# Performance work log

Measured on AMD Instinct MI355X. Metric: run time of the kernel, lower is better.

Reference implementation:

```python
import jax, jax.numpy as jnp
import numpy as np

DEPTH = 10
LEAF = 2 ** DEPTH          # 1024 leaves
NODE_NUM = 2 * LEAF - 1    # 2047
N = NODE_NUM + 1           # 2048 nodes incl. global node 0
ATTN = 4
D = 128
B = 8
L = 2


def _trace_children(ni):
    terms = []
    s, e = ni << 1, (ni << 1) | 1
    while s <= NODE_NUM and e <= NODE_NUM:
        terms.extend(range(s, e + 1))
        s <<= 1
        e = (e << 1) | 1
    return terms


def _trace_left(si):
    ni, cd, terms, stop = si + LEAF, DEPTH, [], False
    while not stop:
        cs = ni - ATTN + 1 - ((ni - ATTN + 1) & 1)
        stop = cs < 2 ** cd
        cs = max(2 ** cd, cs)
        terms.extend(range(cs, ni + 1))
        ni = (cs - 1) >> 1
        cd -= 1
    return terms


def _trace_right(ei):
    ni, cd, terms, stop = ei + LEAF, DEPTH, [], False
    while not stop:
        ce = ni + ATTN - 1 + ((ni - ATTN) & 1)
        stop = ce >= 2 ** (cd + 1)
        ce = min(2 ** (cd + 1) - 1, ce)
        terms.extend(range(ni, ce + 1))
        ni = (ce + 1) >> 1
        cd -= 1
    return terms


def _build_edges():
    src, dst = [], []
    for ni in range(1, NODE_NUM + 1):
        if ni < LEAF:
            t = _trace_children(ni)
        else:
            t = _trace_left(ni - LEAF) + _trace_right(ni - LEAF)
        src.extend(t)
        dst.extend([ni] * len(t))
    e = np.stack([np.asarray(src, np.int64), np.asarray(dst, np.int64)])  # [2, E]
    off = np.arange(B, dtype=np.int64) * N
    eb = (e[:, None, :] + off[None, :, None]).reshape(2, -1)  # batch-offset like _fetch_edge_data
    return eb.astype(np.int32)


def setup_inputs() -> dict:
    key = jax.random.key(0)
    k0, k1, k2 = jax.random.split(key, 3)
    s = 1.0 / np.sqrt(D)
    return {
        "elements": jax.random.normal(k0, (B, LEAF, D), jnp.float32),
        "ln_gamma": jnp.ones((L, D), jnp.float32),
        "ln_beta": jnp.zeros((L, D), jnp.float32),
        "w_nei": (jax.random.normal(k1, (L, D, D), jnp.float32) * s),
        "b_nei": jnp.zeros((L, D), jnp.float32),
        "w_root": (jax.random.normal(k2, (L, D, D), jnp.float32) * s),
        "edge_index": jnp.asarray(_build_edges()),
    }


def _sinusoid(pos, d):
    # ArbitraryPositionEncoder: sinusoidal encoding over (possibly negative) positions
    half = d // 2
    inv = jnp.exp(-jnp.arange(half, dtype=jnp.float32) * (np.log(10000.0) / half))
    ang = pos[:, None] * inv[None, :]  # [n, half]
    return jnp.stack([jnp.sin(ang), jnp.cos(ang)], -1).reshape(pos.shape[0], d)


def reference(elements, ln_gamma, ln_beta, w_nei, b_nei, w_root, edge_index):
    Bx, leaf, d = elements.shape
    depth = int(np.log2(leaf))
    # bottom-up tree compression (mean of two children)
    cur = elements
    levels = [cur]
    for _ in range(depth):
        cur = 0.5 * (cur[:, 0::2] + cur[:, 1::2])
        levels.append(cur)
    # node ordering: [global node 0 (=-1), root (level 0), ..., leaves (level depth)]
    node_feat = jnp.concatenate(
        [jnp.full((Bx, 1, d), -1.0, elements.dtype)] + levels[::-1], axis=1)  # [B, N, D]
    n = node_feat.shape[1]
    # positional encoding: vertical = floor(log2(idx)), horizontal = idx - 2^vertical
    idx = jnp.arange(n, dtype=jnp.float32)
    vpos = jnp.floor(jnp.log2(jnp.where(idx == 0, 0.5, idx)))
    hpos = idx - jnp.exp2(vpos)
    enc = jnp.concatenate([_sinusoid(hpos, d // 2), _sinusoid(vpos, d // 2)], -1)  # [N, D]
    x = (node_feat + enc[None]).reshape(Bx * n, d)
    src, dst = edge_index[0], edge_index[1]
    nseg = Bx * n
    deg = jnp.maximum(
        jax.ops.segment_sum(jnp.ones(src.shape, jnp.float32), dst, num_segments=nseg), 1.0)
    # DeepGCNLayer res+ blocks with SAGEConv (mean aggr)
    for l in range(ln_gamma.shape[0]):
        mu = jnp.mean(x, -1, keepdims=True)
        var = jnp.mean((x - mu) ** 2, -1, keepdims=True)
        h = (x - mu) * jax.lax.rsqrt(var + 1e-5) * ln_gamma[l] + ln_beta[l]
        h = jax.nn.gelu(h, approximate=False)
        agg = jax.ops.segment_sum(h[src], dst, num_segments=nseg) / deg[:, None]
        h = agg @ w_nei[l] + b_nei[l] + h @ w_root[l]
        x = x + h
    return x.reshape(Bx, n, d)
```

## Files before the change

### kernel.cpp

```cpp
#include <hip/hip_runtime.h>
#include <hip/hip_bf16.h>

#define LEAFN 1024
#define NN    2048
#define BATCH 8
#define DD    128
#define ROWS  (BATCH*NN)
#define AHS   384
#define NB    256
#define NT    1024

#define LOG1E4_OVER_32 0.28782313662425575f

#define SLACK 9
#define CSTRIDE 136
#define AGGL_OFF 54672
#define RED_OFF  63376
#define RED2_OFF 64400

typedef __bf16 bf16x8 __attribute__((ext_vector_type(8)));
typedef float  floatx4 __attribute__((ext_vector_type(4)));
typedef float  floatx2 __attribute__((ext_vector_type(2)));

__device__ __forceinline__ float bf2f(unsigned short u) {
  return __uint_as_float(((unsigned)u) << 16);
}
__device__ __forceinline__ unsigned short f2bf(float f) {
  unsigned u = __float_as_uint(f);
  u += 0x7FFFu + ((u >> 16) & 1u);
  return (unsigned short)(u >> 16);
}
__device__ __forceinline__ float gelu(float v) {
  return 0.5f * v * (1.0f + erff(v * 0.70710678118f));
}
__device__ __forceinline__ floatx2 bfpair(unsigned u) {
  floatx2 r;
  r[0] = __uint_as_float(u << 16);
  r[1] = __uint_as_float(u & 0xffff0000u);
  return r;
}

__device__ __forceinline__ float enc_val(int node, int d) {
  float hp, vp;
  if (node == 0) { hp = -0.5f; vp = -1.0f; }
  else {
    int v = 31 - __clz(node);
    hp = (float)(node - (1 << v));
    vp = (float)v;
  }
  float pos = (d < 64) ? hp : vp;
  int i = ((d < 64) ? d : (d - 64)) >> 1;
  float inv = __expf(-(float)i * LOG1E4_OVER_32);
  float ang = pos * inv;
  return (d & 1) ? __cosf(ang) : __sinf(ang);
}

__device__ __forceinline__ void win_cd(int jb, int cd, int& lo_, int& wd_) {
  int g0 = 1024 + jb * 32, g1 = g0 + 31;
  int a0 = g0 >> (10 - cd), a1 = g1 >> (10 - cd);
  int l = a0 - SLACK, h = a1 + SLACK;
  int lvlo = 1 << cd, lvhi = (2 << cd) - 1;
  lo_ = l < lvlo ? lvlo : l;
  int hh = h > lvhi ? lvhi : h;
  int w = hh - lo_ + 1;
  wd_ = w < 0 ? 0 : w;
}

__device__ __forceinline__ void gbarN(int* bar, int slot) {
  __syncthreads();
  if (threadIdx.x == 0) {
    int g = blockIdx.x & 7;
    int* base = bar + (slot * 8 + g) * 64;
    __threadfence();
    if (__hip_atomic_fetch_add(base, 1, __ATOMIC_RELAXED,
                               __HIP_MEMORY_SCOPE_AGENT) == 31)
      __hip_atomic_store(base + 32, 1, __ATOMIC_RELAXED,
                         __HIP_MEMORY_SCOPE_AGENT);
    while (!__hip_atomic_load(base + 32, __ATOMIC_RELAXED,
                              __HIP_MEMORY_SCOPE_AGENT))
      __builtin_amdgcn_s_sleep(1);
    __threadfence();
  }
  __syncthreads();
}

__device__ __forceinline__ void ph_tree(char* smemc, int b, int s,
                                        const float* __restrict__ elements,
                                        float* __restrict__ x,
                                        float* __restrict__ lvl4,
                                        unsigned short* __restrict__ ah,
                                        const float* __restrict__ gamma,
                                        const float* __restrict__ beta,
                                        float* __restrict__ sroot,
                                        float* xci, int* bar) {
  float* sm = (float*)smemc;
  floatx4* smv = (floatx4*)smemc;
  int tid = threadIdx.x;
  const float4* src = (const float4*)(elements + (size_t)(b * LEAFN + s * 64) * DD);
  for (int i = tid; i < 2048; i += NT) {
    int f = i * 4;
    int j = f >> 7, d = f & 127;
    *(float4*)&sm[(63 + j) * DD + d] = src[i];
  }
  __syncthreads();
  for (int lv = 5; lv >= 0; --lv) {
    int nodes = 1 << lv;
    for (int idx = tid; idx < nodes * 32; idx += NT) {
      int k = nodes + (idx >> 5);
      int j = idx & 31;
      smv[(k - 1) * 32 + j] = 0.5f * (smv[(2 * k - 1) * 32 + j] + smv[(2 * k) * 32 + j]);
    }
    __syncthreads();
  }
  if (tid < 32) ((floatx4*)&lvl4[(size_t)(b * 16 + s) * DD])[tid] = smv[tid];
  __syncthreads();
  if (tid == 0) {
    __threadfence();
    __hip_atomic_store(bar + 1536 + b * 64 + s * 4, 1, __ATOMIC_RELAXED,
                       __HIP_MEMORY_SCOPE_AGENT);
  }
  {
    int d2 = tid & 63;
    int i = d2 & 31;
    float inv = __expf(-(float)i * LOG1E4_OVER_32);
    bool lowhalf = d2 < 32;
    for (int idx2 = tid; idx2 < 127 * 64; idx2 += NT) {
      int row = idx2 >> 6;
      int k = row + 1;
      int lv = 31 - __clz(k);
      int g = ((16 + s) << lv) | (k - (1 << lv));
      float vp = (float)(lv + 4);
      float hp = (float)(g - (16 << lv));
      float pos = lowhalf ? hp : vp;
      float sv, cv;
      __sincosf(pos * inv, &sv, &cv);
      int base = row * DD + 2 * d2;
      float xv0 = sm[base] + sv;
      float xv1 = sm[base + 1] + cv;
      sm[base] = xv0; sm[base + 1] = xv1;
      if (k >= 64 || k <= 32) {
        float2 o = make_float2(xv0, xv1);
        *(float2*)&x[((size_t)(b * NN + g)) * DD + 2 * d2] = o;
      }
    }
  }
  __syncthreads();
  {
    int wave = tid >> 6, lane = tid & 63;
    if (wave >= 8) {
      int wl = wave & 7;
      int mt = wl >> 2, nq = wl & 3;
      int m = lane & 15, q = lane >> 4;
#pragma unroll
      for (int ci = 0; ci < 2; ++ci)
#pragma unroll
        for (int r = 0; r < 4; ++r) {
          int t = 32 + mt * 16 + q * 4 + r;
          int k = (t == 63) ? 1 : t + 1;
          int d = (nq * 2 + ci) * 16 + m;
          xci[ci * 4 + r] = sm[(k - 1) * DD + d];
        }
    }
  }
  __syncthreads();
  {
    int sub = tid & 7, dp = sub * 16;
    for (int rr = tid >> 3; rr < 127; rr += NT / 8) {
      float* rowp = &sm[rr * DD + dp];
      float4 q0 = *(float4*)rowp;
      float4 q1 = *(float4*)(rowp + 4);
      float4 q2 = *(float4*)(rowp + 8);
      float4 q3 = *(float4*)(rowp + 12);
      float v[16] = {q0.x, q0.y, q0.z, q0.w, q1.x, q1.y, q1.z, q1.w,
                     q2.x, q2.y, q2.z, q2.w, q3.x, q3.y, q3.z, q3.w};
      float s1 = 0.f, s2 = 0.f;
#pragma unroll
      for (int j = 0; j < 16; ++j) { s1 += v[j]; s2 += v[j] * v[j]; }
      s1 += __shfl_xor(s1, 1); s2 += __shfl_xor(s2, 1);
      s1 += __shfl_xor(s1, 2); s2 += __shfl_xor(s2, 2);
      s1 += __shfl_xor(s1, 4); s2 += __shfl_xor(s2, 4);
      float mu = s1 * (1.0f / 128.0f);
      float var = s2 * (1.0f / 128.0f) - mu * mu;
      float rinv = rsqrtf(var + 1e-5f);
      int k = rr + 1, lv = 31 - __clz(k);
      int g = ((16 + s) << lv) | (k - (1 << lv));
      __attribute__((aligned(16))) unsigned short o[16];
      float hv[16];
#pragma unroll
      for (int j = 0; j < 16; ++j) {
        hv[j] = gelu((v[j] - mu) * rinv * gamma[dp + j] + beta[dp + j]);
        o[j] = f2bf(hv[j]);
      }
      *(float4*)rowp        = make_float4(hv[0], hv[1], hv[2], hv[3]);
      *(float4*)(rowp + 4)  = make_float4(hv[4], hv[5], hv[6], hv[7]);
      *(float4*)(rowp + 8)  = make_float4(hv[8], hv[9], hv[10], hv[11]);
      *(float4*)(rowp + 12) = make_float4(hv[12], hv[13], hv[14], hv[15]);
      unsigned short* dst = &ah[(size_t)(b * NN + g) * AHS + 128 + dp];
      *(uint4*)&dst[0] = *(uint4*)&o[0];
      *(uint4*)&dst[8] = *(uint4*)&o[8];
    }
  }
  __syncthreads();
  for (int lv = 5; lv >= 0; --lv) {
    int nk = 1 << lv;
    float inv = 1.0f / (float)((1 << (7 - lv)) - 2);
    for (int idx = tid; idx < nk * 32; idx += NT) {
      int k = nk + (idx >> 5);
      int j = idx & 31;
      floatx4 S = smv[(2 * k - 1) * 32 + j] + smv[(2 * k) * 32 + j];
      if (lv < 5) S = S + smv[(4 * k - 1) * 32 + j] + smv[(4 * k + 1) * 32 + j];
      smv[(2 * k - 1) * 32 + j] = S;
      int g = ((16 + s) << lv) | (k - nk);
      ushort4 o;
      o.x = f2bf(S[0] * inv); o.y = f2bf(S[1] * inv);
      o.z = f2bf(S[2] * inv); o.w = f2bf(S[3] * inv);
      *(ushort4*)&ah[(size_t)(b * NN + g) * AHS + j * 4] = o;
    }
    __syncthreads();
  }
  if (tid < 32)
    ((floatx4*)&sroot[(size_t)(b * 16 + s) * DD])[tid] = smv[32 + tid];
}

__device__ __forceinline__ void ph_top(char* smemc, int b,
                                       const float* __restrict__ lvl4,
                                       unsigned short* __restrict__ ah,
                                       const float* __restrict__ gamma,
                                       const float* __restrict__ beta) {
  float (*xs)[DD] = (float(*)[DD])smemc;
  int tid = threadIdx.x;
  if (tid < 128) {
    int d = tid;
    float v[16];
    for (int j = 0; j < 16; ++j) v[j] = lvl4[(b * 16 + j) * DD + d];
    for (int j = 0; j < 8; ++j) v[j] = 0.5f * (v[2 * j] + v[2 * j + 1]);
    for (int j = 0; j < 8; ++j) xs[8 + j][d] = v[j] + enc_val(8 + j, d);
    for (int j = 0; j < 4; ++j) v[j] = 0.5f * (v[2 * j] + v[2 * j + 1]);
    for (int j = 0; j < 4; ++j) xs[4 + j][d] = v[j] + enc_val(4 + j, d);
    for (int j = 0; j < 2; ++j) v[j] = 0.5f * (v[2 * j] + v[2 * j + 1]);
    for (int j = 0; j < 2; ++j) xs[2 + j][d] = v[j] + enc_val(2 + j, d);
    v[0] = 0.5f * (v[0] + v[1]);
    xs[1][d] = v[0] + enc_val(1, d);
    xs[0][d] = -1.0f + enc_val(0, d);
  }
  __syncthreads();
  if (tid < 128) {
    int rr = tid >> 3, sub = tid & 7, dp = sub * 16;
    float w[16], s1 = 0.f, s2 = 0.f;
#pragma unroll
    for (int j = 0; j < 16; ++j) { w[j] = xs[rr][dp + j]; s1 += w[j]; s2 += w[j] * w[j]; }
    s1 += __shfl_xor(s1, 1); s2 += __shfl_xor(s2, 1);
    s1 += __shfl_xor(s1, 2); s2 += __shfl_xor(s2, 2);
    s1 += __shfl_xor(s1, 4); s2 += __shfl_xor(s2, 4);
    float mu = s1 * (1.0f / 128.0f);
    float var = s2 * (1.0f / 128.0f) - mu * mu;
    float rinv = rsqrtf(var + 1e-5f);
    __attribute__((aligned(16))) unsigned short o[16];
#pragma unroll
    for (int j = 0; j < 16; ++j)
      o[j] = f2bf(gelu((w[j] - mu) * rinv * gamma[dp + j] + beta[dp + j]));
    unsigned short* dst = &ah[(size_t)(b * NN + rr) * AHS + 128 + dp];
    *(uint4*)&dst[0] = *(uint4*)&o[0];
    *(uint4*)&dst[8] = *(uint4*)&o[8];
  }
  __syncthreads();
}

__device__ __forceinline__ void ph_aggsub(char* smemc, int b, int s,
                                          unsigned short* ah,
                                          float* __restrict__ sroot) {
  floatx4 (*S)[32] = (floatx4(*)[32])smemc;
  int tid = threadIdx.x;
  for (int idx = tid; idx < 32 * 32; idx += NT) {
    int k = 32 + (idx >> 5), q = idx & 31;
    int c = (16 + s) * 64 + (2 * k - 64);
    size_t a0 = (size_t)(b * NN + c) * AHS + 256 + q * 4;
    ushort4 u0 = *(const ushort4*)&ah[a0];
    ushort4 u1 = *(const ushort4*)&ah[a0 + AHS];
    floatx4 v;
    v[0] = bf2f(u0.x) + bf2f(u1.x);
    v[1] = bf2f(u0.y) + bf2f(u1.y);
    v[2] = bf2f(u0.z) + bf2f(u1.z);
    v[3] = bf2f(u0.w) + bf2f(u1.w);
    S[k][q] = v;
    int g = (16 + s) * 32 + (k - 32);
    int r = b * NN + g;
    ushort4 o;
    o.x = f2bf(v[0] * 0.5f); o.y = f2bf(v[1] * 0.5f);
    o.z = f2bf(v[2] * 0.5f); o.w = f2bf(v[3] * 0.5f);
    *(ushort4*)&ah[(size_t)r * AHS + q * 4] = o;
  }
  __syncthreads();
  for (int lv = 4; lv >= 0; --lv) {
    int nk = 1 << lv;
    float inv = 1.0f / (float)((1 << (7 - lv)) - 2);
    for (int idx = tid; idx < nk * 32; idx += NT) {
      int k = nk + (idx >> 5), q = idx & 31;
      int c = ((16 + s) << (lv + 1)) | (2 * k - 2 * nk);
      size_t a0 = (size_t)(b * NN + c) * AHS + 256 + q * 4;
      ushort4 u0 = *(const ushort4*)&ah[a0];
      ushort4 u1 = *(const ushort4*)&ah[a0 + AHS];
      floatx4 sc0 = S[2 * k][q], sc1 = S[2 * k + 1][q];
      floatx4 v;
      v[0] = bf2f(u0.x) + bf2f(u1.x) + sc0[0] + sc1[0];
      v[1] = bf2f(u0.y) + bf2f(u1.y) + sc0[1] + sc1[1];
      v[2] = bf2f(u0.z) + bf2f(u1.z) + sc0[2] + sc1[2];
      v[3] = bf2f(u0.w) + bf2f(u1.w) + sc0[3] + sc1[3];
      S[k][q] = v;
      int g = ((16 + s) << lv) | (k - nk);
      int r = b * NN + g;
      ushort4 o;
      o.x = f2bf(v[0] * inv); o.y = f2bf(v[1] * inv);
      o.z = f2bf(v[2] * inv); o.w = f2bf(v[3] * inv);
      *(ushort4*)&ah[(size_t)r * AHS + q * 4] = o;
    }
    __syncthreads();
  }
  for (int q = tid; q < 32; q += NT)
    ((floatx4*)sroot)[(size_t)(b * 16 + s) * 32 + q] = S[1][q];
}

__device__ __forceinline__ void ph_leafagg(char* smemc, int b, int jb,
                                           const int* __restrict__ srcv,
                                           const int* __restrict__ s0a,
                                           const int* __restrict__ s1a,
                                           const unsigned short* __restrict__ eoff,
                                           unsigned short* ah, int hoff) {
  unsigned short* cache = (unsigned short*)smemc;
  int tid = threadIdx.x;
  int lo[11], wd[11], off[11];
  int acc_off = 0;
#pragma unroll
  for (int cd = 10; cd >= 1; --cd) {
    win_cd(jb, cd, lo[cd], wd[cd]);
    off[cd] = acc_off;
    acc_off += wd[cd];
  }
#pragma unroll
  for (int cd = 10; cd >= 1; --cd) {
    int w = wd[cd];
    for (int t = tid; t < w * 16; t += NT) {
      int row = t >> 4, seg = t & 15;
      *(uint4*)&cache[(off[cd] + row) * CSTRIDE + seg * 8] =
          *(const uint4*)&ah[(size_t)(b * NN + lo[cd] + row) * AHS + hoff + seg * 8];
    }
  }
  __syncthreads();

  int leaf = tid >> 5, half = (tid >> 4) & 1, c = tid & 15;
  int r = b * NN + 1024 + jb * 32 + leaf;
  int e0 = s0a[r], e1 = s1a[r];
  int n = e1 - e0;
  int mid = e0 + (n >> 1);
  int ebeg = half ? mid : e0;
  int eend = half ? e1 : mid;
  int cb = c * 16;
  floatx2 a0 = {0.f, 0.f}, a1 = {0.f, 0.f}, a2 = {0.f, 0.f}, a3 = {0.f, 0.f};
  auto one = [&](int ei) {
    unsigned o = eoff[ei];
    uint4 u;
    if (o != 0xFFFFu)
      u = *(const uint4*)(smemc + o + cb);
    else {
      int g = srcv[ei] - b * NN;
      u = *(const uint4*)&ah[(size_t)(b * NN + g) * AHS + hoff + c * 8];
    }
    a0 += bfpair(u.x); a1 += bfpair(u.y); a2 += bfpair(u.z); a3 += bfpair(u.w);
  };
  int e = ebeg;
  for (; e + 4 <= eend; e += 4) {
    unsigned o0 = eoff[e], o1 = eoff[e + 1], o2 = eoff[e + 2], o3 = eoff[e + 3];
    if (!((((o0 + 1) | (o1 + 1) | (o2 + 1) | (o3 + 1)) >> 16))) {
      uint4 u0 = *(const uint4*)(smemc + o0 + cb);
      uint4 u1 = *(const uint4*)(smemc + o1 + cb);
      uint4 u2 = *(const uint4*)(smemc + o2 + cb);
      uint4 u3 = *(const uint4*)(smemc + o3 + cb);
      a0 += bfpair(u0.x); a1 += bfpair(u0.y); a2 += bfpair(u0.z); a3 += bfpair(u0.w);
      a0 += bfpair(u1.x); a1 += bfpair(u1.y); a2 += bfpair(u1.z); a3 += bfpair(u1.w);
      a0 += bfpair(u2.x); a1 += bfpair(u2.y); a2 += bfpair(u2.z); a3 += bfpair(u2.w);
      a0 += bfpair(u3.x); a1 += bfpair(u3.y); a2 += bfpair(u3.z); a3 += bfpair(u3.w);
    } else {
      one(e); one(e + 1); one(e + 2); one(e + 3);
    }
  }
  for (; e < eend; ++e) one(e);
  a0[0] += __shfl_xor(a0[0], 16); a0[1] += __shfl_xor(a0[1], 16);
  a1[0] += __shfl_xor(a1[0], 16); a1[1] += __shfl_xor(a1[1], 16);
  a2[0] += __shfl_xor(a2[0], 16); a2[1] += __shfl_xor(a2[1], 16);
  a3[0] += __shfl_xor(a3[0], 16); a3[1] += __shfl_xor(a3[1], 16);
  if (!half) {
    float inv = 1.0f / (float)max(n, 1);
    unsigned short* aggl = (unsigned short*)(smemc + AGGL_OFF);
    __attribute__((aligned(16))) unsigned short o[8];
    o[0] = f2bf(a0[0] * inv); o[1] = f2bf(a0[1] * inv);
    o[2] = f2bf(a1[0] * inv); o[3] = f2bf(a1[1] * inv);
    o[4] = f2bf(a2[0] * inv); o[5] = f2bf(a2[1] * inv);
    o[6] = f2bf(a3[0] * inv); o[7] = f2bf(a3[1] * inv);
    *(uint4*)&aggl[leaf * CSTRIDE + c * 8] = *(uint4*)&o[0];
  }
}

__device__ __forceinline__ void ph_topfin(int b,
                                          const float* __restrict__ sroot,
                                          unsigned short* ah, int hoff) {
  int d = threadIdx.x;
  float S16[16], h16[16], Sv[16];
#pragma unroll
  for (int j = 0; j < 16; ++j) S16[j] = sroot[(size_t)(b * 16 + j) * DD + d];
#pragma unroll
  for (int j = 0; j < 16; ++j)
    h16[j] = bf2f(ah[(size_t)(b * NN + 16 + j) * AHS + hoff + d]);
#pragma unroll
  for (int k = 8; k < 16; ++k)
    Sv[k] = h16[2 * k - 16] + h16[2 * k - 15] + S16[2 * k - 16] + S16[2 * k - 15];
#pragma unroll
  for (int k = 7; k >= 1; --k)
    Sv[k] = bf2f(ah[(size_t)(b * NN + 2 * k) * AHS + hoff + d]) +
            bf2f(ah[(size_t)(b * NN + 2 * k + 1) * AHS + hoff + d]) +
            Sv[2 * k] + Sv[2 * k + 1];
#pragma unroll
  for (int k = 1; k < 16; ++k) {
    int dv = 31 - __clz(k);
    float inv = 1.0f / (float)((1 << (11 - dv)) - 2);
    ah[(size_t)(b * NN + k) * AHS + d] = f2bf(Sv[k] * inv);
  }
  ah[(size_t)(b * NN) * AHS + d] = f2bf(0.0f);
}

__device__ __forceinline__ void ph_gemm32(char* redc, const unsigned short* aggl,
                                          int rowbase, unsigned short* ah,
                                          const unsigned short* __restrict__ wfl,
                                          const float* __restrict__ bn,
                                          float* __restrict__ x, int hoff_in,
                                          const float* __restrict__ gamma,
                                          const float* __restrict__ beta,
                                          float* xc, int first_layer) {
  int wave = threadIdx.x >> 6, lane = threadIdx.x & 63;
  bool act = wave < 8;
  int wl = wave & 7;
  int mt = wl >> 2, nq = wl & 3;
  int r0 = rowbase + mt * 16;
  int m = lane & 15, q = lane >> 4;
  floatx4 acc[2];
  acc[0] = (floatx4){0.f, 0.f, 0.f, 0.f};
  acc[1] = (floatx4){0.f, 0.f, 0.f, 0.f};
  if (act) {
    const unsigned short* arow = ah + (size_t)(r0 + m) * AHS + q * 8;
    const bf16x8* B = (const bf16x8*)wfl + lane;
#pragma unroll
    for (int kc = 0; kc < 8; ++kc) {
      bf16x8 a0;
      if (kc < 4)
        a0 = *(const bf16x8*)&aggl[(mt * 16 + m) * CSTRIDE + kc * 32 + q * 8];
      else
        a0 = *(const bf16x8*)(arow + hoff_in + (kc - 4) * 32);
#pragma unroll
      for (int ci = 0; ci < 2; ++ci) {
        bf16x8 bb = B[(kc * 8 + nq * 2 + ci) * 64];
        acc[ci] = __builtin_amdgcn_mfma_f32_16x16x32_bf16(a0, bb, acc[ci], 0, 0, 0);
      }
    }
  }
  if (first_layer) {
    float s1[4] = {0.f, 0.f, 0.f, 0.f}, s2[4] = {0.f, 0.f, 0.f, 0.f};
    if (act) {
#pragma unroll
      for (int ci = 0; ci < 2; ++ci) {
        int col = (nq * 2 + ci) * 16 + m;
        float bias = bn[col];
#pragma unroll
        for (int r = 0; r < 4; ++r) {
          int row = r0 + q * 4 + r;
          float v = x[(size_t)row * DD + col] + acc[ci][r] + bias;
          xc[ci * 4 + r] = v;
          s1[r] += v; s2[r] += v * v;
        }
      }
#pragma unroll
      for (int r = 0; r < 4; ++r) {
        s1[r] += __shfl_xor(s1[r], 1); s2[r] += __shfl_xor(s2[r], 1);
        s1[r] += __shfl_xor(s1[r], 2); s2[r] += __shfl_xor(s2[r], 2);
        s1[r] += __shfl_xor(s1[r], 4); s2[r] += __shfl_xor(s2[r], 4);
        s1[r] += __shfl_xor(s1[r], 8); s2[r] += __shfl_xor(s2[r], 8);
      }
    }
    float* red = (float*)redc;
    int rl = mt * 16 + q * 4;
    __syncthreads();
    if (act && m == 0) {
#pragma unroll
      for (int r = 0; r < 4; ++r) {
        red[(rl + r) * 4 + nq] = s1[r];
        red[128 + (rl + r) * 4 + nq] = s2[r];
      }
    }
    __syncthreads();
    if (act) {
      float mu[4], rv[4];
#pragma unroll
      for (int r = 0; r < 4; ++r) {
        float t1 = red[(rl + r) * 4] + red[(rl + r) * 4 + 1] +
                   red[(rl + r) * 4 + 2] + red[(rl + r) * 4 + 3];
        float t2 = red[128 + (rl + r) * 4] + red[128 + (rl + r) * 4 + 1] +
                   red[128 + (rl + r) * 4 + 2] + red[128 + (rl + r) * 4 + 3];
        mu[r] = t1 * (1.0f / 128.0f);
        float var = t2 * (1.0f / 128.0f) - mu[r] * mu[r];
        rv[r] = rsqrtf(var + 1e-5f);
      }
#pragma unroll
      for (int ci = 0; ci < 2; ++ci) {
        int col = (nq * 2 + ci) * 16 + m;
        float gm = gamma[col], bt = beta[col];
#pragma unroll
        for (int r = 0; r < 4; ++r) {
          int row = r0 + q * 4 + r;
          float hh = gelu((xc[ci * 4 + r] - mu[r]) * rv[r] * gm + bt);
          ah[(size_t)row * AHS + 256 + col] = f2bf(hh);
        }
      }
    }
  } else {
    if (act) {
#pragma unroll
      for (int ci = 0; ci < 2; ++ci) {
        int col = (nq * 2 + ci) * 16 + m;
        float bias = bn[col];
#pragma unroll
        for (int r = 0; r < 4; ++r) {
          int row = r0 + q * 4 + r;
          x[(size_t)row * DD + col] = xc[ci * 4 + r] + acc[ci][r] + bias;
        }
      }
    }
  }
}

__device__ __forceinline__ void ph_gemm32s(char* redc, int b, int sb, int tbase,
                                           unsigned short* ah,
                                           const unsigned short* __restrict__ wfl,
                                           const float* __restrict__ bn,
                                           float* __restrict__ x, int hoff_in,
                                           const float* __restrict__ gamma,
                                           const float* __restrict__ beta,
                                           float* xc, int first_layer,
                                           const float* __restrict__ gx) {
  int wave = threadIdx.x >> 6, lane = threadIdx.x & 63;
  bool act = wave >= 8;
  int wl = wave & 7;
  int mt = wl >> 2, nq = wl & 3;
  int m = lane & 15, q = lane >> 4;
  int tA = tbase + mt * 16 + m;
  int kA = (tA == 63) ? 1 : tA + 1;
  int lvA = 31 - __clz(kA);
  int rowA = b * NN + (((16 + sb) << lvA) | (kA - (1 << lvA)));
  int rowO[4];
#pragma unroll
  for (int r = 0; r < 4; ++r) {
    int t = tbase + mt * 16 + q * 4 + r;
    int k = (t == 63) ? 1 : t + 1;
    int lv = 31 - __clz(k);
    rowO[r] = b * NN + (((16 + sb) << lv) | (k - (1 << lv)));
  }
  floatx4 acc[2];
  acc[0] = (floatx4){0.f, 0.f, 0.f, 0.f};
  acc[1] = (floatx4){0.f, 0.f, 0.f, 0.f};
  if (act) {
    const unsigned short* arow = ah + (size_t)rowA * AHS + q * 8;
    const bf16x8* B = (const bf16x8*)wfl + lane;
#pragma unroll
    for (int kc = 0; kc < 8; ++kc) {
      int koff = (kc < 4) ? kc * 32 : hoff_in + (kc - 4) * 32;
      bf16x8 a0 = *(const bf16x8*)(arow + koff);
#pragma unroll
      for (int ci = 0; ci < 2; ++ci) {
        bf16x8 bb = B[(kc * 8 + nq * 2 + ci) * 64];
        acc[ci] = __builtin_amdgcn_mfma_f32_16x16x32_bf16(a0, bb, acc[ci], 0, 0, 0);
      }
    }
  }
  if (first_layer) {
    float s1[4] = {0.f, 0.f, 0.f, 0.f}, s2[4] = {0.f, 0.f, 0.f, 0.f};
    if (act) {
#pragma unroll
      for (int ci = 0; ci < 2; ++ci) {
        int col = (nq * 2 + ci) * 16 + m;
        float bias = bn[col];
#pragma unroll
        for (int r = 0; r < 4; ++r) {
          float x0 = gx ? gx[(size_t)rowO[r] * DD + col] : xc[ci * 4 + r];
          float v = x0 + acc[ci][r] + bias;
          xc[ci * 4 + r] = v;
          s1[r] += v; s2[r] += v * v;
        }
      }
#pragma unroll
      for (int r = 0; r < 4; ++r) {
        s1[r] += __shfl_xor(s1[r], 1); s2[r] += __shfl_xor(s2[r], 1);
        s1[r] += __shfl_xor(s1[r], 2); s2[r] += __shfl_xor(s2[r], 2);
        s1[r] += __shfl_xor(s1[r], 4); s2[r] += __shfl_xor(s2[r], 4);
        s1[r] += __shfl_xor(s1[r], 8); s2[r] += __shfl_xor(s2[r], 8);
      }
    }
    float* red = (float*)redc;
    int rl = mt * 16 + q * 4;
    __syncthreads();
    if (act && m == 0) {
#pragma unroll
      for (int r = 0; r < 4; ++r) {
        red[(rl + r) * 4 + nq] = s1[r];
        red[128 + (rl + r) * 4 + nq] = s2[r];
      }
    }
    __syncthreads();
    if (act) {
      float mu[4], rv[4];
#pragma unroll
      for (int r = 0; r < 4; ++r) {
        float t1 = red[(rl + r) * 4] + red[(rl + r) * 4 + 1] +
                   red[(rl + r) * 4 + 2] + red[(rl + r) * 4 + 3];
        float t2 = red[128 + (rl + r) * 4] + red[128 + (rl + r) * 4 + 1] +
                   red[128 + (rl + r) * 4 + 2] + red[128 + (rl + r) * 4 + 3];
        mu[r] = t1 * (1.0f / 128.0f);
        float var = t2 * (1.0f / 128.0f) - mu[r] * mu[r];
        rv[r] = rsqrtf(var + 1e-5f);
      }
#pragma unroll
      for (int ci = 0; ci < 2; ++ci) {
        int col = (nq * 2 + ci) * 16 + m;
        float gm = gamma[col], bt = beta[col];
#pragma unroll
        for (int r = 0; r < 4; ++r) {
          float hh = gelu((xc[ci * 4 + r] - mu[r]) * rv[r] * gm + bt);
          ah[(size_t)rowO[r] * AHS + 256 + col] = f2bf(hh);
        }
      }
    }
  } else {
    if (act) {
#pragma unroll
      for (int ci = 0; ci < 2; ++ci) {
        int col = (nq * 2 + ci) * 16 + m;
        float bias = bn[col];
#pragma unroll
        for (int r = 0; r < 4; ++r)
          x[(size_t)rowO[r] * DD + col] = xc[ci * 4 + r] + acc[ci][r] + bias;
      }
    }
  }
}

__device__ __forceinline__ void ph_gemm16t(char* redc, int b,
                                           unsigned short* ah,
                                           const unsigned short* __restrict__ wfl,
                                           const float* __restrict__ bn,
                                           float* __restrict__ x, int hoff_in,
                                           const float* __restrict__ gamma,
                                           const float* __restrict__ beta,
                                           float* xc, int first_layer) {
  int ct = threadIdx.x >> 6, lane = threadIdx.x & 63;
  bool act = ct < 8;
  int m = lane & 15, q = lane >> 4;
  floatx4 acc = (floatx4){0.f, 0.f, 0.f, 0.f};
  int col = (ct & 7) * 16 + m;
  if (act) {
    const unsigned short* arow = ah + (size_t)(b * NN + m) * AHS + q * 8;
    const bf16x8* B = (const bf16x8*)wfl + lane;
#pragma unroll
    for (int kc = 0; kc < 8; ++kc) {
      int koff = (kc < 4) ? kc * 32 : hoff_in + (kc - 4) * 32;
      bf16x8 a0 = *(const bf16x8*)(arow + koff);
      bf16x8 bb = B[(kc * 8 + ct) * 64];
      acc = __builtin_amdgcn_mfma_f32_16x16x32_bf16(a0, bb, acc, 0, 0, 0);
    }
  }
  if (first_layer) {
    float s1[4] = {0.f, 0.f, 0.f, 0.f}, s2[4] = {0.f, 0.f, 0.f, 0.f};
    float bias = act ? bn[col] : 0.f;
    if (act) {
#pragma unroll
      for (int r = 0; r < 4; ++r) {
        float v = xc[r] + acc[r] + bias;
        xc[r] = v; s1[r] = v; s2[r] = v * v;
      }
#pragma unroll
      for (int r = 0; r < 4; ++r) {
        s1[r] += __shfl_xor(s1[r], 1); s2[r] += __shfl_xor(s2[r], 1);
        s1[r] += __shfl_xor(s1[r], 2); s2[r] += __shfl_xor(s2[r], 2);
        s1[r] += __shfl_xor(s1[r], 4); s2[r] += __shfl_xor(s2[r], 4);
        s1[r] += __shfl_xor(s1[r], 8); s2[r] += __shfl_xor(s2[r], 8);
      }
    }
    float* red = (float*)redc;
    __syncthreads();
    if (act && m == 0) {
#pragma unroll
      for (int r = 0; r < 4; ++r) {
        red[(q * 4 + r) * 8 + ct] = s1[r];
        red[128 + (q * 4 + r) * 8 + ct] = s2[r];
      }
    }
    __syncthreads();
    if (act) {
#pragma unroll
      for (int r = 0; r < 4; ++r) {
        float t1 = 0.f, t2 = 0.f;
#pragma unroll
        for (int j = 0; j < 8; ++j) {
          t1 += red[(q * 4 + r) * 8 + j];
          t2 += red[128 + (q * 4 + r) * 8 + j];
        }
        float mu = t1 * (1.0f / 128.0f);
        float var = t2 * (1.0f / 128.0f) - mu * mu;
        float rv = rsqrtf(var + 1e-5f);
        float hh = gelu((xc[r] - mu) * rv * gamma[col] + beta[col]);
        ah[(size_t)(b * NN + q * 4 + r) * AHS + 256 + col] = f2bf(hh);
      }
    }
  } else {
    if (act) {
      float bias = bn[col];
#pragma unroll
      for (int r = 0; r < 4; ++r)
        x[(size_t)(b * NN + q * 4 + r) * DD + col] = xc[r] + acc[r] + bias;
    }
  }
}

__global__ __launch_bounds__(NT, 1) void k_mega(
    const float* __restrict__ elements, const float* __restrict__ ln_gamma,
    const float* __restrict__ ln_beta, const float* __restrict__ w_nei,
    const float* __restrict__ b_nei, const float* __restrict__ w_root,
    const int* __restrict__ srcv, const int* __restrict__ dstv, int E,
    float* __restrict__ x, int* s0a, int* s1a, float* lvl4, float* sroot,
    unsigned short* wf, unsigned short* ah, unsigned short* eoff, int* bar) {
  __shared__ __align__(16) char smem[65536];
  int bid = blockIdx.x, tid = threadIdx.x;
  int b = bid & 7, gb = bid >> 3;
  int Eb = E >> 3;
  unsigned short* wfg = wf + (size_t)b * 65536;
  float xcl[8], xci[8], xct[4];
  int wv = tid >> 6;

  if (gb < 16) {
    ph_tree(smem, b, gb, elements, x, lvl4, ah, ln_gamma, ln_beta, sroot, xci, bar);
  } else if (gb < 24) {
    int base = b * Eb;
    for (int i = base + (gb - 16) * NT + tid; i < base + Eb; i += 8 * NT) {
      int dv = dstv[i];
      if (i == 0 || dstv[i - 1] != dv) s0a[dv] = i;
      if (i == base + Eb - 1 || dstv[i + 1] != dv) s1a[dv] = i + 1;
    }
    for (int i = base + (gb - 16) * NT + tid; i < base + Eb; i += 8 * NT) {
      int dl = dstv[i] - b * NN - 1024;
      unsigned short ov = 0xFFFFu;
      if (dl >= 0) {
        int jb2 = dl >> 5;
        int g = srcv[i] - b * NN;
        int lv = 31 - __clz(g);
        int acc2 = 0;
#pragma unroll
        for (int cd = 10; cd >= 1; --cd) {
          int lo_, wd_;
          win_cd(jb2, cd, lo_, wd_);
          if (cd == lv) {
            int idx = g - lo_;
            if ((unsigned)idx < (unsigned)wd_)
              ov = (unsigned short)((acc2 + idx) * (2 * CSTRIDE));
          }
          acc2 += wd_;
        }
      }
      eoff[i] = ov;
    }
  } else if (gb < 28) {
    int gi = (gb - 24) * NT + tid;
    int lane = gi & 63, ct = (gi >> 6) & 7, kc = gi >> 9;
    int n = ct * 16 + (lane & 15);
    int k = kc * 32 + (lane >> 4) * 8;
    int kk = k & 127;
#pragma unroll
    for (int l = 0; l < 2; ++l) {
      const float* w = (k < 128) ? (w_nei + (size_t)l * DD * DD)
                                 : (w_root + (size_t)l * DD * DD);
      unsigned short* o = wfg + (size_t)l * 32768 + (size_t)gi * 8;
#pragma unroll
      for (int j = 0; j < 8; ++j) o[j] = f2bf(w[(size_t)(kk + j) * DD + n]);
    }
  } else if (gb == 28) {
    if (tid < 16) {
      while (!__hip_atomic_load(bar + 1536 + b * 64 + tid * 4, __ATOMIC_RELAXED,
                                __HIP_MEMORY_SCOPE_AGENT))
        __builtin_amdgcn_s_sleep(1);
      __threadfence();
    }
    __syncthreads();
    ph_top(smem, b, lvl4, ah, ln_gamma, ln_beta);
    {
      int ln = tid & 63, m_ = ln & 15, q_ = ln >> 4;
      if (wv < 8) {
        float (*xs)[DD] = (float(*)[DD])smem;
#pragma unroll
        for (int r = 0; r < 4; ++r) xct[r] = xs[q_ * 4 + r][wv * 16 + m_];
      }
    }
  }
  gbarN(bar, 0);

  if (gb == 28) {
    if (tid < 128) ph_topfin(b, sroot, ah, 128);
    __syncthreads();
    ph_gemm16t(smem + RED_OFF, b, ah, wfg, b_nei, x, 128,
               ln_gamma + DD, ln_beta + DD, xct, 1);
    __syncthreads();
  }
  ph_leafagg(smem, b, gb, srcv, s0a, s1a, eoff, ah, 128);
  __syncthreads();
  if (wv < 8) {
    ph_gemm32(smem + RED_OFF, (const unsigned short*)(smem + AGGL_OFF),
              b * NN + 1024 + gb * 32, ah, wfg, b_nei, x, 128,
              ln_gamma + DD, ln_beta + DD, xcl, 1);
  } else if (gb < 16) {
    ph_gemm32s(smem + RED2_OFF, b, gb, 32, ah, wfg, b_nei, x, 128,
               ln_gamma + DD, ln_beta + DD, xci, 1, nullptr);
  } else {
    ph_gemm32s(smem + RED2_OFF, b, gb - 16, 0, ah, wfg, b_nei, x, 128,
               ln_gamma + DD, ln_beta + DD, xci, 1, x);
  }
  gbarN(bar, 1);

  if (gb < 16) {
    ph_aggsub(smem, b, gb, ah, sroot);
    __syncthreads();
    if (tid == 0) {
      __threadfence();
      __hip_atomic_store(bar + 1024 + b * 64 + gb * 4, 1, __ATOMIC_RELAXED,
                         __HIP_MEMORY_SCOPE_AGENT);
    }
  }
  ph_leafagg(smem, b, gb, srcv, s0a, s1a, eoff, ah, 256);
  if (gb >= 16 && tid == 0) {
    while (!__hip_atomic_load(bar + 1024 + b * 64 + (gb - 16) * 4, __ATOMIC_RELAXED,
                              __HIP_MEMORY_SCOPE_AGENT))
      __builtin_amdgcn_s_sleep(1);
    __threadfence();
  }
  __syncthreads();
  if (wv < 8) {
    ph_gemm32(smem + RED_OFF, (const unsigned short*)(smem + AGGL_OFF),
              b * NN + 1024 + gb * 32, ah, wfg + 32768, b_nei + DD,
              x, 256, ln_gamma, ln_beta, xcl, 0);
  } else if (gb < 16) {
    ph_gemm32s(smem + RED2_OFF, b, gb, 32, ah, wfg + 32768, b_nei + DD, x, 256,
               ln_gamma, ln_beta, xci, 0, nullptr);
  } else {
    ph_gemm32s(smem + RED2_OFF, b, gb - 16, 0, ah, wfg + 32768, b_nei + DD, x, 256,
               ln_gamma, ln_beta, xci, 0, nullptr);
  }
  if (gb == 28) {
    if (tid < 16) {
      while (!__hip_atomic_load(bar + 1024 + b * 64 + tid * 4, __ATOMIC_RELAXED,
                                __HIP_MEMORY_SCOPE_AGENT))
        __builtin_amdgcn_s_sleep(1);
      __threadfence();
    }
    __syncthreads();
    if (tid < 128) ph_topfin(b, sroot, ah, 256);
    __syncthreads();
    ph_gemm16t(smem + RED_OFF, b, ah, wfg + 32768, b_nei + DD, x, 256,
               ln_gamma, ln_beta, xct, 0);
  }
}

extern "C" void kernel_launch(void* const* d_in, const int* in_sizes, int n_in,
                              void* d_out, int out_size, void* d_ws, size_t ws_size,
                              hipStream_t stream) {
  const float* elements = (const float*)d_in[0];
  const float* ln_gamma = (const float*)d_in[1];
  const float* ln_beta  = (const float*)d_in[2];
  const float* w_nei    = (const float*)d_in[3];
  const float* b_nei    = (const float*)d_in[4];
  const float* w_root   = (const float*)d_in[5];
  const int*   edge     = (const int*)d_in[6];
  int E = in_sizes[6] / 2;
  const int* srcv = edge;
  const int* dstv = edge + E;
  float* x = (float*)d_out;

  char* ws = (char*)d_ws;
  int*            bar   = (int*)ws;
  int*            s0    = (int*)(ws + 65536);
  int*            s1    = (int*)(ws + 131072);
  float*          lvl4  = (float*)(ws + 196608);
  float*          sroot = (float*)(ws + 262144);
  unsigned short* wf    = (unsigned short*)(ws + 327680);
  unsigned short* ah    = (unsigned short*)(ws + 327680 + 1048576);
  unsigned short* eoff  = (unsigned short*)(ws + 327680 + 1048576 + 12582912);

  hipMemsetAsync(bar, 0, 8192, stream);
  k_mega<<<dim3(NB), dim3(NT), 0, stream>>>(
      elements, ln_gamma, ln_beta, w_nei, b_nei, w_root,
      srcv, dstv, E, x, s0, s1, lvl4, sroot, wf, ah, eoff, bar);
}
```

Baseline: 163.4 us.

## Compute leaf neighbor aggregation as sparse-matrix MFMA over cached window rows

Replaces the per-edge gather-and-add leaf aggregation with a dense 0/1 selection matrix built in shared memory, multiplied on MFMA against a transposed cache of the window rows, processed in two K-chunks. Edges whose source falls outside the cached window are flagged per leaf and handled by a scalar fallback path. This trades irregular LDS gathers for regular matrix-core work, but adds shared-memory zeroing, scattered 16-bit transposed stores, and extra barriers.

```diff
diff --git a/kernel.cpp b/kernel.cpp
--- a/kernel.cpp
+++ b/kernel.cpp
@@ -14,6 +14,12 @@
 
 #define SLACK 9
 #define CSTRIDE 136
+#define SB_OFF   0
+#define SBT      520
+#define S_OFF    33280
+#define SSTR     232
+#define DEG_OFF  48128
+#define FB_OFF   48256
 #define AGGL_OFF 54672
 #define RED_OFF  63376
 #define RED2_OFF 64400
@@ -322,12 +328,20 @@
 
 __device__ __forceinline__ void ph_leafagg(char* smemc, int b, int jb,
                                            const int* __restrict__ srcv,
+                                           const int* __restrict__ dstv,
                                            const int* __restrict__ s0a,
                                            const int* __restrict__ s1a,
                                            const unsigned short* __restrict__ eoff,
                                            unsigned short* ah, int hoff) {
-  unsigned short* cache = (unsigned short*)smemc;
   int tid = threadIdx.x;
+  int lane = tid & 63, wv = tid >> 6;
+  unsigned short* SB = (unsigned short*)(smemc + SB_OFF);
+  unsigned short* S  = (unsigned short*)(smemc + S_OFF);
+  float* invdeg = (float*)(smemc + DEG_OFF);
+  unsigned int* fb = (unsigned int*)(smemc + FB_OFF);
+  unsigned short* aggl = (unsigned short*)(smemc + AGGL_OFF);
+  int rbase = b * NN + 1024 + jb * 32;
+
   int lo[11], wd[11], off[11];
   int acc_off = 0;
 #pragma unroll
@@ -336,67 +350,116 @@
     off[cd] = acc_off;
     acc_off += wd[cd];
   }
+
+  for (int t = tid; t < 48128 / 16; t += NT)
+    ((uint4*)smemc)[t] = make_uint4(0, 0, 0, 0);
+  if (tid < 32)
+    invdeg[tid] = 1.0f / (float)max(s1a[rbase + tid] - s0a[rbase + tid], 1);
+  if (tid == 0) *fb = 0u;
+  __syncthreads();
+
+  {
+    int E0 = s0a[rbase], E1 = s1a[rbase + 31];
+    for (int e = E0 + tid; e < E1; e += NT) {
+      int leaf = dstv[e] - rbase;
+      unsigned kr = eoff[e];
+      if (kr == 0xFFFFu) atomicOr(fb, 1u << leaf);
+      else S[leaf * SSTR + kr] = 0x3F80;
+    }
+  }
 #pragma unroll
   for (int cd = 10; cd >= 1; --cd) {
     int w = wd[cd];
     for (int t = tid; t < w * 16; t += NT) {
       int row = t >> 4, seg = t & 15;
-      *(uint4*)&cache[(off[cd] + row) * CSTRIDE + seg * 8] =
-          *(const uint4*)&ah[(size_t)(b * NN + lo[cd] + row) * AHS + hoff + seg * 8];
-    }
-  }
-  __syncthreads();
-
-  int leaf = tid >> 5, half = (tid >> 4) & 1, c = tid & 15;
-  int r = b * NN + 1024 + jb * 32 + leaf;
-  int e0 = s0a[r], e1 = s1a[r];
-  int n = e1 - e0;
-  int mid = e0 + (n >> 1);
-  int ebeg = half ? mid : e0;
-  int eend = half ? e1 : mid;
-  int cb = c * 16;
-  floatx2 a0 = {0.f, 0.f}, a1 = {0.f, 0.f}, a2 = {0.f, 0.f}, a3 = {0.f, 0.f};
-  auto one = [&](int ei) {
-    unsigned o = eoff[ei];
-    uint4 u;
-    if (o != 0xFFFFu)
-      u = *(const uint4*)(smemc + o + cb);
-    else {
-      int g = srcv[ei] - b * NN;
-      u = *(const uint4*)&ah[(size_t)(b * NN + g) * AHS + hoff + c * 8];
-    }
-    a0 += bfpair(u.x); a1 += bfpair(u.y); a2 += bfpair(u.z); a3 += bfpair(u.w);
-  };
-  int e = ebeg;
-  for (; e + 4 <= eend; e += 4) {
-    unsigned o0 = eoff[e], o1 = eoff[e + 1], o2 = eoff[e + 2], o3 = eoff[e + 3];
-    if (!((((o0 + 1) | (o1 + 1) | (o2 + 1) | (o3 + 1)) >> 16))) {
-      uint4 u0 = *(const uint4*)(smemc + o0 + cb);
-      uint4 u1 = *(const uint4*)(smemc + o1 + cb);
-      uint4 u2 = *(const uint4*)(smemc + o2 + cb);
-      uint4 u3 = *(const uint4*)(smemc + o3 + cb);
-      a0 += bfpair(u0.x); a1 += bfpair(u0.y); a2 += bfpair(u0.z); a3 += bfpair(u0.w);
-      a0 += bfpair(u1.x); a1 += bfpair(u1.y); a2 += bfpair(u1.z); a3 += bfpair(u1.w);
-      a0 += bfpair(u2.x); a1 += bfpair(u2.y); a2 += bfpair(u2.z); a3 += bfpair(u2.w);
-      a0 += bfpair(u3.x); a1 += bfpair(u3.y); a2 += bfpair(u3.z); a3 += bfpair(u3.w);
-    } else {
-      one(e); one(e + 1); one(e + 2); one(e + 3);
-    }
-  }
-  for (; e < eend; ++e) one(e);
-  a0[0] += __shfl_xor(a0[0], 16); a0[1] += __shfl_xor(a0[1], 16);
-  a1[0] += __shfl_xor(a1[0], 16); a1[1] += __shfl_xor(a1[1], 16);
-  a2[0] += __shfl_xor(a2[0], 16); a2[1] += __shfl_xor(a2[1], 16);
-  a3[0] += __shfl_xor(a3[0], 16); a3[1] += __shfl_xor(a3[1], 16);
-  if (!half) {
-    float inv = 1.0f / (float)max(n, 1);
-    unsigned short* aggl = (unsigned short*)(smemc + AGGL_OFF);
-    __attribute__((aligned(16))) unsigned short o[8];
-    o[0] = f2bf(a0[0] * inv); o[1] = f2bf(a0[1] * inv);
-    o[2] = f2bf(a1[0] * inv); o[3] = f2bf(a1[1] * inv);
-    o[4] = f2bf(a2[0] * inv); o[5] = f2bf(a2[1] * inv);
-    o[6] = f2bf(a3[0] * inv); o[7] = f2bf(a3[1] * inv);
-    *(uint4*)&aggl[leaf * CSTRIDE + c * 8] = *(uint4*)&o[0];
+      int kr = off[cd] + row;
+      if (kr >= 128) continue;
+      uint4 u = *(const uint4*)&ah[(size_t)(b * NN + lo[cd] + row) * AHS + hoff + seg * 8];
+      int krl = kr;
+      unsigned short* p = SB + ((krl >> 5) * 8 + (seg >> 1)) * SBT +
+                          ((krl & 31) >> 3) * 128 + (seg & 1) * 64 + (krl & 7);
+      p[0]  = (unsigned short)(u.x & 0xffff);
+      p[8]  = (unsigned short)(u.x >> 16);
+      p[16] = (unsigned short)(u.y & 0xffff);
+      p[24] = (unsigned short)(u.y >> 16);
+      p[32] = (unsigned short)(u.z & 0xffff);
+      p[40] = (unsigned short)(u.z >> 16);
+      p[48] = (unsigned short)(u.w & 0xffff);
+      p[56] = (unsigned short)(u.w >> 16);
+    }
+  }
+  __syncthreads();
+
+  int m = lane & 15, q = lane >> 4;
+  int mt = wv >> 3, nt = wv & 7;
+  floatx4 acc = (floatx4){0.f, 0.f, 0.f, 0.f};
+#pragma unroll
+  for (int kcl = 0; kcl < 4; ++kcl) {
+    bf16x8 a0 = *(const bf16x8*)&S[(mt * 16 + m) * SSTR + kcl * 32 + q * 8];
+    bf16x8 bb = *(const bf16x8*)&SB[(kcl * 8 + nt) * SBT + lane * 8];
+    acc = __builtin_amdgcn_mfma_f32_16x16x32_bf16(a0, bb, acc, 0, 0, 0);
+  }
+  __syncthreads();
+
+  for (int t = tid; t < 24 * SBT / 8; t += NT)
+    ((uint4*)SB)[t] = make_uint4(0, 0, 0, 0);
+  __syncthreads();
+
+#pragma unroll
+  for (int cd = 10; cd >= 1; --cd) {
+    int w = wd[cd];
+    for (int t = tid; t < w * 16; t += NT) {
+      int row = t >> 4, seg = t & 15;
+      int kr = off[cd] + row;
+      if (kr < 128) continue;
+      uint4 u = *(const uint4*)&ah[(size_t)(b * NN + lo[cd] + row) * AHS + hoff + seg * 8];
+      int krl = kr - 128;
+      unsigned short* p = SB + ((krl >> 5) * 8 + (seg >> 1)) * SBT +
+                          ((krl & 31) >> 3) * 128 + (seg & 1) * 64 + (krl & 7);
+      p[0]  = (unsigned short)(u.x & 0xffff);
+      p[8]  = (unsigned short)(u.x >> 16);
+      p[16] = (unsigned short)(u.y & 0xffff);
+      p[24] = (unsigned short)(u.y >> 16);
+      p[32] = (unsigned short)(u.z & 0xffff);
+      p[40] = (unsigned short)(u.z >> 16);
+      p[48] = (unsigned short)(u.w & 0xffff);
+      p[56] = (unsigned short)(u.w >> 16);
+    }
+  }
+  __syncthreads();
+
+#pragma unroll
+  for (int kcl = 0; kcl < 3; ++kcl) {
+    bf16x8 a0 = *(const bf16x8*)&S[(mt * 16 + m) * SSTR + (4 + kcl) * 32 + q * 8];
+    bf16x8 bb = *(const bf16x8*)&SB[(kcl * 8 + nt) * SBT + lane * 8];
+    acc = __builtin_amdgcn_mfma_f32_16x16x32_bf16(a0, bb, acc, 0, 0, 0);
+  }
+#pragma unroll
+  for (int r = 0; r < 4; ++r) {
+    int leaf = mt * 16 + q * 4 + r;
+    aggl[leaf * CSTRIDE + nt * 16 + m] = f2bf(acc[r] * invdeg[leaf]);
+  }
+  __syncthreads();
+
+  unsigned fbm = *fb;
+  if (fbm && tid < 512) {
+    int leaf = tid >> 4, c = tid & 15;
+    if ((fbm >> leaf) & 1) {
+      int e0 = s0a[rbase + leaf], e1 = s1a[rbase + leaf];
+      floatx2 a0 = {0.f, 0.f}, a1 = {0.f, 0.f}, a2 = {0.f, 0.f}, a3 = {0.f, 0.f};
+      for (int e = e0; e < e1; ++e) {
+        int g = srcv[e] - b * NN;
+        uint4 u = *(const uint4*)&ah[(size_t)(b * NN + g) * AHS + hoff + c * 8];
+        a0 += bfpair(u.x); a1 += bfpair(u.y); a2 += bfpair(u.z); a3 += bfpair(u.w);
+      }
+      float inv = 1.0f / (float)max(e1 - e0, 1);
+      __attribute__((aligned(16))) unsigned short o[8];
+      o[0] = f2bf(a0[0] * inv); o[1] = f2bf(a0[1] * inv);
+      o[2] = f2bf(a1[0] * inv); o[3] = f2bf(a1[1] * inv);
+      o[4] = f2bf(a2[0] * inv); o[5] = f2bf(a2[1] * inv);
+      o[6] = f2bf(a3[0] * inv); o[7] = f2bf(a3[1] * inv);
+      *(uint4*)&aggl[leaf * CSTRIDE + c * 8] = *(uint4*)&o[0];
+    }
   }
 }
 
@@ -765,7 +828,7 @@
           if (cd == lv) {
             int idx = g - lo_;
             if ((unsigned)idx < (unsigned)wd_)
-              ov = (unsigned short)((acc2 + idx) * (2 * CSTRIDE));
+              ov = (unsigned short)(acc2 + idx);
           }
           acc2 += wd_;
         }
@@ -813,7 +876,7 @@
                ln_gamma + DD, ln_beta + DD, xct, 1);
     __syncthreads();
   }
-  ph_leafagg(smem, b, gb, srcv, s0a, s1a, eoff, ah, 128);
+  ph_leafagg(smem, b, gb, srcv, dstv, s0a, s1a, eoff, ah, 128);
   __syncthreads();
   if (wv < 8) {
     ph_gemm32(smem + RED_OFF, (const unsigned short*)(smem + AGGL_OFF),
@@ -837,7 +900,7 @@
                          __HIP_MEMORY_SCOPE_AGENT);
     }
   }
-  ph_leafagg(smem, b, gb, srcv, s0a, s1a, eoff, ah, 256);
+  ph_leafagg(smem, b, gb, srcv, dstv, s0a, s1a, eoff, ah, 256);
   if (gb >= 16 && tid == 0) {
     while (!__hip_atomic_load(bar + 1024 + b * 64 + (gb - 16) * 4, __ATOMIC_RELAXED,
                               __HIP_MEMORY_SCOPE_AGENT))
```

Result: no change. 160.7 us (-1.6%).
